# Kernel tuning notes

Hardware: AMD Instinct MI355X
Metric: run time of the kernel (lower is better)

The kernel has to match this reference:

```python
import math
import jax, jax.numpy as jnp
import numpy as np

NUM_EMBED = 2048
EMBED_FEATS = 64
IN_FEATS = 512
B, T = 16, 4096
COMMITMENT_COST = 0.25


def setup_inputs() -> dict:
    key = jax.random.key(0)
    k1, k2, k3, k4 = jax.random.split(key, 4)
    x = jax.random.normal(k1, (B, IN_FEATS, T), dtype=jnp.float32)
    proj_w = jax.random.normal(k2, (EMBED_FEATS, IN_FEATS), dtype=jnp.float32) / np.sqrt(IN_FEATS)
    proj_b = jax.random.normal(k3, (EMBED_FEATS,), dtype=jnp.float32) * 0.01
    embed = jax.random.normal(k4, (NUM_EMBED, EMBED_FEATS), dtype=jnp.float32)
    return {"x": x, "proj_w": proj_w, "proj_b": proj_b, "embed": embed}


def reference(x, proj_w, proj_b, embed):
    # 1x1 Conv1d projection, then transpose(1,-1): [B, Cin, T] -> [B, T, E]
    h = jnp.einsum('ec,bct->bte', proj_w, x) + proj_b  # [B, T, E]
    Bb, Tt, E = h.shape
    K = embed.shape[0]
    flat = h.reshape(-1, E)  # [N, E]
    # squared distances to codewords: [N, K]
    d2 = (jnp.sum(flat * flat, axis=1, keepdims=True)
          + jnp.sum(embed * embed, axis=1)
          - 2.0 * flat @ embed.T)
    q_idx = jnp.argmin(d2, axis=1)  # [N]
    z_q = embed[q_idx].reshape(Bb, Tt, E)  # one-hot @ embed == gather
    # commitment loss (codebook updated by EMA, so only commitment term)
    commitment = jnp.mean((jax.lax.stop_gradient(z_q) - h) ** 2)
    loss = COMMITMENT_COST * commitment
    # straight-through estimator
    z_q_st = h + jax.lax.stop_gradient(z_q - h)
    # code usage stats
    N = flat.shape[0]
    probs = jnp.zeros((K,), dtype=jnp.float32).at[q_idx].add(1.0) / N
    log_perplexity = -jnp.sum(probs * jnp.log(probs + 1e-10))
    kldiv_r = math.log(K) * (N / Bb) * jnp.ones((Bb, 1), dtype=jnp.float32)
    z_q_out = jnp.swapaxes(z_q_st, 1, 2)  # [B, E, T]
    return z_q_out, loss, kldiv_r, log_perplexity
```

## Files before the change

kernel.cpp:

```cpp
#include <hip/hip_runtime.h>
#include <math.h>

#define B_ 16
#define T_ 4096
#define C_ 512
#define E_ 64
#define K_ 2048
#define N_ (B_*T_)
#define ZQ_ELEMS 4194304

typedef __attribute__((ext_vector_type(8))) short short8;
typedef __attribute__((ext_vector_type(4))) short short4v;
typedef __attribute__((ext_vector_type(4))) float f32x4;

#define WS_EHI   0
#define WS_ELO   262144
#define WS_NHCC  524288
#define WS_WHI   532480
#define WS_WLO   598016
#define WS_QIDX  663552
#define WS_HIST  925696
#define WS_LOSS  933888

struct HiLo { short hi, lo; };

__device__ __forceinline__ unsigned short rne16(float v) {
    unsigned u = __float_as_uint(v);
    return (unsigned short)((u + 0x7FFFu + ((u >> 16) & 1u)) >> 16);
}
__device__ __forceinline__ HiLo split_rne(float v) {
    HiLo r;
    unsigned hb = rne16(v);
    r.hi = (short)hb;
    float hf = __uint_as_float((unsigned)hb << 16);
    r.lo = (short)rne16(v - hf);
    return r;
}

__global__ void prep_kernel(const float* __restrict__ embed,
                            const float* __restrict__ W,
                            short* __restrict__ ehi, short* __restrict__ elo,
                            float* __restrict__ nhcc,
                            short* __restrict__ whi, short* __restrict__ wlo) {
    const int tid = threadIdx.x;
    if (blockIdx.x < 64) {
        const int row = blockIdx.x * 32 + (tid >> 3);
        const int c = (tid & 7) * 8;
        const float* src = embed + (size_t)row * 64 + c;
        short8 hv, lv;
        float s = 0.f;
#pragma unroll
        for (int j = 0; j < 8; ++j) {
            float v = src[j];
            s = fmaf(v, v, s);
            HiLo r = split_rne(v);
            hv[j] = r.hi; lv[j] = r.lo;
        }
        *(short8*)(ehi + (size_t)row * 64 + c) = hv;
        *(short8*)(elo + (size_t)row * 64 + c) = lv;
        s += __shfl_xor(s, 1, 64);
        s += __shfl_xor(s, 2, 64);
        s += __shfl_xor(s, 4, 64);
        if ((tid & 7) == 0) nhcc[row] = -0.5f * s;
    } else {
        int idx = ((blockIdx.x - 64) * 256 + tid) * 4;
        float4 v = *(const float4*)(W + idx);
        short4v h, l;
        HiLo a = split_rne(v.x); h[0] = a.hi; l[0] = a.lo;
        HiLo b = split_rne(v.y); h[1] = b.hi; l[1] = b.lo;
        HiLo c = split_rne(v.z); h[2] = c.hi; l[2] = c.lo;
        HiLo d = split_rne(v.w); h[3] = d.hi; l[3] = d.lo;
        *(short4v*)(whi + idx) = h;
        *(short4v*)(wlo + idx) = l;
    }
}

__global__ __launch_bounds__(256, 2) void projvq_kernel(
        const float* __restrict__ x,
        const short* __restrict__ whi, const short* __restrict__ wlo,
        const float* __restrict__ bias,
        const short* __restrict__ ehi, const short* __restrict__ elo,
        const float* __restrict__ nhcc,
        int* __restrict__ qidx, int* __restrict__ hist,
        float* __restrict__ lossacc) {
    __shared__ float smemf[8704];
    float* xs = smemf;
    short* hT_hi = (short*)smemf;
    short* hT_lo = hT_hi + 8704;
    short* es_hi = (short*)smemf;
    short* es_lo = es_hi + 8192;
    float* ccs   = (float*)(es_lo + 8192);

    const int tid = threadIdx.x;
    const int wave = tid >> 6, lane = tid & 63;
    const int row16 = lane & 15, quad = lane >> 4;
    const int n0 = blockIdx.x * 128;
    const int b  = n0 / T_;
    const int t0 = n0 % T_;
    const float* xb = x + (size_t)b * C_ * T_ + t0;

    f32x4 acc[2][4];
#pragma unroll
    for (int i = 0; i < 2; ++i)
#pragma unroll
        for (int j = 0; j < 4; ++j) acc[i][j] = (f32x4){0.f, 0.f, 0.f, 0.f};

    for (int c0 = 0; c0 < C_; c0 += 32) {
#pragma unroll
        for (int j = 0; j < 4; ++j) {
            int linear = j * 1024 + tid * 4;
            int cc = linear >> 7, tt = linear & 127;
            float4 v = *(const float4*)(xb + (size_t)(c0 + cc) * T_ + tt);
            *(float4*)(xs + cc * 136 + tt) = v;
        }
        __syncthreads();

        short8 bh[2], bl[2];
#pragma unroll
        for (int tt2 = 0; tt2 < 2; ++tt2) {
            int t = wave * 32 + tt2 * 16 + row16;
#pragma unroll
            for (int j = 0; j < 8; ++j) {
                float v = xs[(quad * 8 + j) * 136 + t];
                HiLo r = split_rne(v);
                bh[tt2][j] = r.hi; bl[tt2][j] = r.lo;
            }
        }

#pragma unroll
        for (int et = 0; et < 4; ++et) {
            size_t aoff = (size_t)(et * 16 + row16) * C_ + c0 + quad * 8;
            short8 ah = *(const short8*)(whi + aoff);
            short8 al = *(const short8*)(wlo + aoff);
#pragma unroll
            for (int tt2 = 0; tt2 < 2; ++tt2) {
                acc[tt2][et] = __builtin_amdgcn_mfma_f32_16x16x32_bf16(ah, bh[tt2], acc[tt2][et], 0, 0, 0);
                acc[tt2][et] = __builtin_amdgcn_mfma_f32_16x16x32_bf16(al, bh[tt2], acc[tt2][et], 0, 0, 0);
                acc[tt2][et] = __builtin_amdgcn_mfma_f32_16x16x32_bf16(ah, bl[tt2], acc[tt2][et], 0, 0, 0);
                acc[tt2][et] = __builtin_amdgcn_mfma_f32_16x16x32_bf16(al, bl[tt2], acc[tt2][et], 0, 0, 0);
            }
        }
        __syncthreads();
    }

    float hh = 0.f;
#pragma unroll
    for (int et = 0; et < 4; ++et) {
        float4 bv = *(const float4*)(bias + et * 16 + quad * 4);
#pragma unroll
        for (int tt2 = 0; tt2 < 2; ++tt2) {
            f32x4 a = acc[tt2][et];
            a[0] += bv.x; a[1] += bv.y; a[2] += bv.z; a[3] += bv.w;
            hh = fmaf(a[0], a[0], hh); hh = fmaf(a[1], a[1], hh);
            hh = fmaf(a[2], a[2], hh); hh = fmaf(a[3], a[3], hh);
            short4v hv, lv;
#pragma unroll
            for (int r = 0; r < 4; ++r) {
                HiLo sp = split_rne(a[r]);
                hv[r] = sp.hi; lv[r] = sp.lo;
            }
            int t = wave * 32 + tt2 * 16 + row16;
            int e0 = et * 16 + quad * 4;
            *(short4v*)(hT_hi + t * 68 + e0) = hv;
            *(short4v*)(hT_lo + t * 68 + e0) = lv;
        }
    }
#pragma unroll
    for (int m = 1; m < 64; m <<= 1) hh += __shfl_xor(hh, m, 64);
    if (lane == 0) atomicAdd(lossacc, hh);
    __syncthreads();

    short8 a_hi[2][2], a_lo[2][2];
#pragma unroll
    for (int rt = 0; rt < 2; ++rt)
#pragma unroll
        for (int ks = 0; ks < 2; ++ks) {
            int lr = wave * 32 + rt * 16 + row16;
            a_hi[rt][ks] = *(const short8*)(hT_hi + lr * 68 + ks * 32 + quad * 8);
            a_lo[rt][ks] = *(const short8*)(hT_lo + lr * 68 + ks * 32 + quad * 8);
        }
    __syncthreads();

    const int rs = row16 & 7;
    const int off0 = (quad ^ rs) * 8;

    float vmax[2][4];
    int   vidx[2][4];
#pragma unroll
    for (int rt = 0; rt < 2; ++rt)
#pragma unroll
        for (int rg = 0; rg < 4; ++rg) { vmax[rt][rg] = -3.4e38f; vidx[rt][rg] = 0; }

    for (int k0 = 0; k0 < K_; k0 += 128) {
#pragma unroll
        for (int it = 0; it < 4; ++it) {
            int idx = it * 256 + tid;
            int r = idx >> 3, g = idx & 7;
            int dst = r * 64 + (g ^ (r & 7)) * 8;
            *(short8*)(es_hi + dst) = *(const short8*)(ehi + (size_t)(k0 + r) * 64 + g * 8);
            *(short8*)(es_lo + dst) = *(const short8*)(elo + (size_t)(k0 + r) * 64 + g * 8);
        }
        if (tid < 32) *(f32x4*)(ccs + tid * 4) = *(const f32x4*)(nhcc + k0 + tid * 4);
        __syncthreads();

#pragma unroll
        for (int kt = 0; kt < 8; ++kt) {
            const int row = kt * 16 + row16;
            const float ci = ccs[row];
            const short* p = es_hi + row * 64;
            const short* q = es_lo + row * 64;
            short8 bh0 = *(const short8*)(p + off0);
            short8 bh1 = *(const short8*)(p + (off0 ^ 32));
            short8 bl0 = *(const short8*)(q + off0);
            short8 bl1 = *(const short8*)(q + (off0 ^ 32));
            const int kk = k0 + row;
#pragma unroll
            for (int rt = 0; rt < 2; ++rt) {
                f32x4 acc2 = {ci, ci, ci, ci};
                acc2 = __builtin_amdgcn_mfma_f32_16x16x32_bf16(a_hi[rt][0], bh0, acc2, 0, 0, 0);
                acc2 = __builtin_amdgcn_mfma_f32_16x16x32_bf16(a_hi[rt][1], bh1, acc2, 0, 0, 0);
                acc2 = __builtin_amdgcn_mfma_f32_16x16x32_bf16(a_lo[rt][0], bh0, acc2, 0, 0, 0);
                acc2 = __builtin_amdgcn_mfma_f32_16x16x32_bf16(a_lo[rt][1], bh1, acc2, 0, 0, 0);
                acc2 = __builtin_amdgcn_mfma_f32_16x16x32_bf16(a_hi[rt][0], bl0, acc2, 0, 0, 0);
                acc2 = __builtin_amdgcn_mfma_f32_16x16x32_bf16(a_hi[rt][1], bl1, acc2, 0, 0, 0);
#pragma unroll
                for (int rg = 0; rg < 4; ++rg) {
                    float v = acc2[rg];
                    if (v > vmax[rt][rg]) { vmax[rt][rg] = v; vidx[rt][rg] = kk; }
                }
            }
        }
        __syncthreads();
    }

    float s = 0.f;
#pragma unroll
    for (int rt = 0; rt < 2; ++rt) {
#pragma unroll
        for (int rg = 0; rg < 4; ++rg) {
            float v = vmax[rt][rg];
            int ix = vidx[rt][rg];
#pragma unroll
            for (int m = 1; m < 16; m <<= 1) {
                float ov = __shfl_xor(v, m, 64);
                int   oi = __shfl_xor(ix, m, 64);
                if (ov > v || (ov == v && oi < ix)) { v = ov; ix = oi; }
            }
            if (row16 == 0) {
                int rown = n0 + wave * 32 + rt * 16 + quad * 4 + rg;
                qidx[rown] = ix;
                atomicAdd(&hist[ix], 1);
                s += v;
            }
        }
    }
    s += __shfl_xor(s, 16, 64);
    s += __shfl_xor(s, 32, 64);
    if (lane == 0) atomicAdd(lossacc, -2.f * s);
}

__global__ void gather_kernel(const float* __restrict__ embed,
                              const int* __restrict__ qidx,
                              float* __restrict__ out) {
    __shared__ float tile[64 * 65];
    __shared__ int qs[64];
    const int tid = threadIdx.x;
    const int t0 = blockIdx.x * 64;
    const int b  = blockIdx.y;

    if (tid < 64) qs[tid] = qidx[b * T_ + t0 + tid];
    __syncthreads();

    const int t_l = tid >> 2, eq = tid & 3;
    const float4* src = (const float4*)(embed + (size_t)qs[t_l] * 64 + eq * 16);
#pragma unroll
    for (int j = 0; j < 4; ++j) {
        float4 v = src[j];
        int e = eq * 16 + j * 4;
        tile[t_l * 65 + e + 0] = v.x;
        tile[t_l * 65 + e + 1] = v.y;
        tile[t_l * 65 + e + 2] = v.z;
        tile[t_l * 65 + e + 3] = v.w;
    }
    __syncthreads();

    const int tt = tid & 63;
#pragma unroll
    for (int j = 0; j < 16; ++j) {
        int e = j * 4 + (tid >> 6);
        out[((size_t)b * 64 + e) * T_ + t0 + tt] = tile[tt * 65 + e];
    }
}

__global__ void finalize_kernel(const int* __restrict__ hist,
                                const float* __restrict__ lossacc,
                                float* __restrict__ out) {
    __shared__ float red[4];
    const int tid = threadIdx.x;
    float s = 0.f;
    for (int k = tid; k < K_; k += 256) {
        float p = (float)hist[k] * (1.f / 65536.f);
        s -= p * logf(p + 1e-10f);
    }
#pragma unroll
    for (int m = 1; m < 64; m <<= 1) s += __shfl_xor(s, m, 64);
    if ((tid & 63) == 0) red[tid >> 6] = s;
    __syncthreads();
    if (tid == 0) {
        float lp = red[0] + red[1] + red[2] + red[3];
        out[ZQ_ELEMS] = 0.25f * lossacc[0] / (float)ZQ_ELEMS;
        out[ZQ_ELEMS + 17] = lp;
    }
    if (tid < 16) out[ZQ_ELEMS + 1 + tid] = logf(2048.f) * 4096.f;
}

extern "C" void kernel_launch(void* const* d_in, const int* in_sizes, int n_in,
                              void* d_out, int out_size, void* d_ws, size_t ws_size,
                              hipStream_t stream) {
    const float* x      = (const float*)d_in[0];
    const float* proj_w = (const float*)d_in[1];
    const float* proj_b = (const float*)d_in[2];
    const float* embed  = (const float*)d_in[3];
    float* out = (float*)d_out;
    char* ws = (char*)d_ws;

    short* e_hi = (short*)(ws + WS_EHI);
    short* e_lo = (short*)(ws + WS_ELO);
    float* nhcc = (float*)(ws + WS_NHCC);
    short* w_hi = (short*)(ws + WS_WHI);
    short* w_lo = (short*)(ws + WS_WLO);
    int*   qidx = (int*)(ws + WS_QIDX);
    int*   hist = (int*)(ws + WS_HIST);
    float* lossac = (float*)(ws + WS_LOSS);

    (void)hipMemsetAsync(ws + WS_HIST, 0, K_ * sizeof(int) + sizeof(float), stream);

    prep_kernel<<<96, 256, 0, stream>>>(embed, proj_w, e_hi, e_lo, nhcc, w_hi, w_lo);
    projvq_kernel<<<N_ / 128, 256, 0, stream>>>(x, w_hi, w_lo, proj_b,
                                                e_hi, e_lo, nhcc, qidx, hist, lossac);
    gather_kernel<<<dim3(T_ / 64, B_), 256, 0, stream>>>(embed, qidx, out);
    finalize_kernel<<<1, 256, 0, stream>>>(hist, lossac, out);
}
```

Before: 309.1 us.

## Fuse codebook gather into VQ kernel and prefetch x and codebook tiles

Folds the gather/transpose of chosen codewords into the projection+VQ kernel, so the separate gather launch and the qidx round-trip through global memory go away. The codebook hi/lo copies are stored pre-permuted in MFMA fragment order, so the shared-memory fill and fragment reads become linear. Codebook chunks and x tiles are software-prefetched into registers one iteration ahead to overlap global loads with MFMA work. The bias/norm constant is now added after the MFMA chain. The trade-off is higher register pressure in a kernel launched with two blocks per SM, plus a longer kernel tail.

Result: no change. 305.5 us (-1.2%).

```diff
diff --git a/kernel.cpp b/kernel.cpp
--- a/kernel.cpp
+++ b/kernel.cpp
@@ -18,9 +18,8 @@
 #define WS_NHCC  524288
 #define WS_WHI   532480
 #define WS_WLO   598016
-#define WS_QIDX  663552
-#define WS_HIST  925696
-#define WS_LOSS  933888
+#define WS_HIST  663552
+#define WS_LOSS  671744
 
 struct HiLo { short hi, lo; };
 
@@ -45,8 +44,8 @@
     const int tid = threadIdx.x;
     if (blockIdx.x < 64) {
         const int row = blockIdx.x * 32 + (tid >> 3);
-        const int c = (tid & 7) * 8;
-        const float* src = embed + (size_t)row * 64 + c;
+        const int g = tid & 7;
+        const float* src = embed + (size_t)row * 64 + g * 8;
         short8 hv, lv;
         float s = 0.f;
 #pragma unroll
@@ -56,12 +55,15 @@
             HiLo r = split_rne(v);
             hv[j] = r.hi; lv[j] = r.lo;
         }
-        *(short8*)(ehi + (size_t)row * 64 + c) = hv;
-        *(short8*)(elo + (size_t)row * 64 + c) = lv;
+        const int c128 = row >> 7, r = row & 127;
+        const int kt = r >> 4, col = r & 15, ks = g >> 2, qe = g & 3;
+        const int slot = (kt * 2 + ks) * 64 + qe * 16 + col;
+        *(short8*)(ehi + c128 * 8192 + slot * 8) = hv;
+        *(short8*)(elo + c128 * 8192 + slot * 8) = lv;
         s += __shfl_xor(s, 1, 64);
         s += __shfl_xor(s, 2, 64);
         s += __shfl_xor(s, 4, 64);
-        if ((tid & 7) == 0) nhcc[row] = -0.5f * s;
+        if (g == 0) nhcc[row] = -0.5f * s;
     } else {
         int idx = ((blockIdx.x - 64) * 256 + tid) * 4;
         float4 v = *(const float4*)(W + idx);
@@ -81,39 +83,49 @@
         const float* __restrict__ bias,
         const short* __restrict__ ehi, const short* __restrict__ elo,
         const float* __restrict__ nhcc,
-        int* __restrict__ qidx, int* __restrict__ hist,
-        float* __restrict__ lossacc) {
-    __shared__ float smemf[8704];
-    float* xs = smemf;
-    short* hT_hi = (short*)smemf;
-    short* hT_lo = hT_hi + 8704;
-    short* es_hi = (short*)smemf;
-    short* es_lo = es_hi + 8192;
-    float* ccs   = (float*)(es_lo + 8192);
+        const float* __restrict__ embed, float* __restrict__ out,
+        int* __restrict__ hist, float* __restrict__ lossacc) {
+    __shared__ float smemf[8832];
+    float* xs   = smemf;
+    short* aimg = (short*)smemf;
+    short* es   = (short*)smemf;
+    float* ccs  = (float*)(smemf + 8192);
+    float* tile = smemf;
+    __shared__ int qs[128];
 
     const int tid = threadIdx.x;
     const int wave = tid >> 6, lane = tid & 63;
     const int row16 = lane & 15, quad = lane >> 4;
-    const int n0 = blockIdx.x * 128;
-    const int b  = n0 / T_;
-    const int t0 = n0 % T_;
+    const int b  = blockIdx.x >> 5;
+    const int t0 = (blockIdx.x & 31) * 128;
     const float* xb = x + (size_t)b * C_ * T_ + t0;
 
+    f32x4 cc0 = *(const f32x4*)(nhcc + tid * 8);
+    f32x4 cc1 = *(const f32x4*)(nhcc + tid * 8 + 4);
+
     f32x4 acc[2][4];
 #pragma unroll
     for (int i = 0; i < 2; ++i)
 #pragma unroll
         for (int j = 0; j < 4; ++j) acc[i][j] = (f32x4){0.f, 0.f, 0.f, 0.f};
 
+    const int xcc = tid >> 5;
+    const int xtt = (tid & 31) * 4;
+    float4 xpf[4];
+#pragma unroll
+    for (int j = 0; j < 4; ++j)
+        xpf[j] = *(const float4*)(xb + (size_t)(xcc + j * 8) * T_ + xtt);
+
     for (int c0 = 0; c0 < C_; c0 += 32) {
 #pragma unroll
-        for (int j = 0; j < 4; ++j) {
-            int linear = j * 1024 + tid * 4;
-            int cc = linear >> 7, tt = linear & 127;
-            float4 v = *(const float4*)(xb + (size_t)(c0 + cc) * T_ + tt);
-            *(float4*)(xs + cc * 136 + tt) = v;
-        }
+        for (int j = 0; j < 4; ++j)
+            *(float4*)(xs + (xcc + j * 8) * 136 + xtt) = xpf[j];
         __syncthreads();
+        if (c0 < C_ - 32) {
+#pragma unroll
+            for (int j = 0; j < 4; ++j)
+                xpf[j] = *(const float4*)(xb + (size_t)(c0 + 32 + xcc + j * 8) * T_ + xtt);
+        }
 
         short8 bh[2], bl[2];
 #pragma unroll
@@ -126,7 +138,6 @@
                 bh[tt2][j] = r.hi; bl[tt2][j] = r.lo;
             }
         }
-
 #pragma unroll
         for (int et = 0; et < 4; ++et) {
             size_t aoff = (size_t)(et * 16 + row16) * C_ + c0 + quad * 8;
@@ -159,10 +170,12 @@
                 HiLo sp = split_rne(a[r]);
                 hv[r] = sp.hi; lv[r] = sp.lo;
             }
-            int t = wave * 32 + tt2 * 16 + row16;
-            int e0 = et * 16 + quad * 4;
-            *(short4v*)(hT_hi + t * 68 + e0) = hv;
-            *(short4v*)(hT_lo + t * 68 + e0) = lv;
+            const int ks = et >> 1;
+            const int qe = (et & 1) * 2 + (quad >> 1);
+            const int j0 = (quad & 1) * 4;
+            const int sl = (((wave * 2 + tt2) * 2 + ks) * 64 + qe * 16 + row16) * 8 + j0;
+            *(short4v*)(aimg + sl) = hv;
+            *(short4v*)(aimg + 8192 + sl) = lv;
         }
     }
 #pragma unroll
@@ -175,14 +188,18 @@
     for (int rt = 0; rt < 2; ++rt)
 #pragma unroll
         for (int ks = 0; ks < 2; ++ks) {
-            int lr = wave * 32 + rt * 16 + row16;
-            a_hi[rt][ks] = *(const short8*)(hT_hi + lr * 68 + ks * 32 + quad * 8);
-            a_lo[rt][ks] = *(const short8*)(hT_lo + lr * 68 + ks * 32 + quad * 8);
-        }
-    __syncthreads();
-
-    const int rs = row16 & 7;
-    const int off0 = (quad ^ rs) * 8;
+            int sl = (((wave * 2 + rt) * 2 + ks) * 64 + lane) * 8;
+            a_hi[rt][ks] = *(const short8*)(aimg + sl);
+            a_lo[rt][ks] = *(const short8*)(aimg + 8192 + sl);
+        }
+    __syncthreads();
+
+    short8 pf[8];
+#pragma unroll
+    for (int it = 0; it < 4; ++it) {
+        pf[it]     = *(const short8*)(ehi + (it * 256 + tid) * 8);
+        pf[4 + it] = *(const short8*)(elo + (it * 256 + tid) * 8);
+    }
 
     float vmax[2][4];
     int   vidx[2][4];
@@ -191,41 +208,49 @@
 #pragma unroll
         for (int rg = 0; rg < 4; ++rg) { vmax[rt][rg] = -3.4e38f; vidx[rt][rg] = 0; }
 
-    for (int k0 = 0; k0 < K_; k0 += 128) {
+    for (int c = 0; c < 16; ++c) {
 #pragma unroll
         for (int it = 0; it < 4; ++it) {
-            int idx = it * 256 + tid;
-            int r = idx >> 3, g = idx & 7;
-            int dst = r * 64 + (g ^ (r & 7)) * 8;
-            *(short8*)(es_hi + dst) = *(const short8*)(ehi + (size_t)(k0 + r) * 64 + g * 8);
-            *(short8*)(es_lo + dst) = *(const short8*)(elo + (size_t)(k0 + r) * 64 + g * 8);
-        }
-        if (tid < 32) *(f32x4*)(ccs + tid * 4) = *(const f32x4*)(nhcc + k0 + tid * 4);
+            *(short8*)(es + (it * 256 + tid) * 8)        = pf[it];
+            *(short8*)(es + 8192 + (it * 256 + tid) * 8) = pf[4 + it];
+        }
+        if ((tid >> 4) == c) {
+            int u = tid & 15;
+            *(f32x4*)(ccs + u * 8)     = cc0;
+            *(f32x4*)(ccs + u * 8 + 4) = cc1;
+        }
         __syncthreads();
+        if (c < 15) {
+            const short* sh = ehi + (c + 1) * 8192;
+            const short* sl2 = elo + (c + 1) * 8192;
+#pragma unroll
+            for (int it = 0; it < 4; ++it) {
+                pf[it]     = *(const short8*)(sh + (it * 256 + tid) * 8);
+                pf[4 + it] = *(const short8*)(sl2 + (it * 256 + tid) * 8);
+            }
+        }
 
 #pragma unroll
         for (int kt = 0; kt < 8; ++kt) {
-            const int row = kt * 16 + row16;
-            const float ci = ccs[row];
-            const short* p = es_hi + row * 64;
-            const short* q = es_lo + row * 64;
-            short8 bh0 = *(const short8*)(p + off0);
-            short8 bh1 = *(const short8*)(p + (off0 ^ 32));
-            short8 bl0 = *(const short8*)(q + off0);
-            short8 bl1 = *(const short8*)(q + (off0 ^ 32));
-            const int kk = k0 + row;
+            const float ci = ccs[kt * 16 + row16];
+            const short* pb = es + (kt * 2) * 512;
+            short8 bh0 = *(const short8*)(pb + lane * 8);
+            short8 bh1 = *(const short8*)(pb + 512 + lane * 8);
+            short8 bl0 = *(const short8*)(pb + 8192 + lane * 8);
+            short8 bl1 = *(const short8*)(pb + 8192 + 512 + lane * 8);
+            const int kk = c * 128 + kt * 16 + row16;
 #pragma unroll
             for (int rt = 0; rt < 2; ++rt) {
-                f32x4 acc2 = {ci, ci, ci, ci};
-                acc2 = __builtin_amdgcn_mfma_f32_16x16x32_bf16(a_hi[rt][0], bh0, acc2, 0, 0, 0);
-                acc2 = __builtin_amdgcn_mfma_f32_16x16x32_bf16(a_hi[rt][1], bh1, acc2, 0, 0, 0);
-                acc2 = __builtin_amdgcn_mfma_f32_16x16x32_bf16(a_lo[rt][0], bh0, acc2, 0, 0, 0);
-                acc2 = __builtin_amdgcn_mfma_f32_16x16x32_bf16(a_lo[rt][1], bh1, acc2, 0, 0, 0);
-                acc2 = __builtin_amdgcn_mfma_f32_16x16x32_bf16(a_hi[rt][0], bl0, acc2, 0, 0, 0);
-                acc2 = __builtin_amdgcn_mfma_f32_16x16x32_bf16(a_hi[rt][1], bl1, acc2, 0, 0, 0);
+                f32x4 a2 = {0.f, 0.f, 0.f, 0.f};
+                a2 = __builtin_amdgcn_mfma_f32_16x16x32_bf16(a_hi[rt][0], bh0, a2, 0, 0, 0);
+                a2 = __builtin_amdgcn_mfma_f32_16x16x32_bf16(a_hi[rt][1], bh1, a2, 0, 0, 0);
+                a2 = __builtin_amdgcn_mfma_f32_16x16x32_bf16(a_lo[rt][0], bh0, a2, 0, 0, 0);
+                a2 = __builtin_amdgcn_mfma_f32_16x16x32_bf16(a_lo[rt][1], bh1, a2, 0, 0, 0);
+                a2 = __builtin_amdgcn_mfma_f32_16x16x32_bf16(a_hi[rt][0], bl0, a2, 0, 0, 0);
+                a2 = __builtin_amdgcn_mfma_f32_16x16x32_bf16(a_hi[rt][1], bl1, a2, 0, 0, 0);
 #pragma unroll
                 for (int rg = 0; rg < 4; ++rg) {
-                    float v = acc2[rg];
+                    float v = a2[rg] + ci;
                     if (v > vmax[rt][rg]) { vmax[rt][rg] = v; vidx[rt][rg] = kk; }
                 }
             }
@@ -247,8 +272,7 @@
                 if (ov > v || (ov == v && oi < ix)) { v = ov; ix = oi; }
             }
             if (row16 == 0) {
-                int rown = n0 + wave * 32 + rt * 16 + quad * 4 + rg;
-                qidx[rown] = ix;
+                qs[wave * 32 + rt * 16 + quad * 4 + rg] = ix;
                 atomicAdd(&hist[ix], 1);
                 s += v;
             }
@@ -257,38 +281,28 @@
     s += __shfl_xor(s, 16, 64);
     s += __shfl_xor(s, 32, 64);
     if (lane == 0) atomicAdd(lossacc, -2.f * s);
-}
-
-__global__ void gather_kernel(const float* __restrict__ embed,
-                              const int* __restrict__ qidx,
-                              float* __restrict__ out) {
-    __shared__ float tile[64 * 65];
-    __shared__ int qs[64];
-    const int tid = threadIdx.x;
-    const int t0 = blockIdx.x * 64;
-    const int b  = blockIdx.y;
-
-    if (tid < 64) qs[tid] = qidx[b * T_ + t0 + tid];
-    __syncthreads();
-
-    const int t_l = tid >> 2, eq = tid & 3;
-    const float4* src = (const float4*)(embed + (size_t)qs[t_l] * 64 + eq * 16);
-#pragma unroll
-    for (int j = 0; j < 4; ++j) {
-        float4 v = src[j];
-        int e = eq * 16 + j * 4;
-        tile[t_l * 65 + e + 0] = v.x;
-        tile[t_l * 65 + e + 1] = v.y;
-        tile[t_l * 65 + e + 2] = v.z;
-        tile[t_l * 65 + e + 3] = v.w;
-    }
-    __syncthreads();
-
-    const int tt = tid & 63;
-#pragma unroll
-    for (int j = 0; j < 16; ++j) {
-        int e = j * 4 + (tid >> 6);
-        out[((size_t)b * 64 + e) * T_ + t0 + tt] = tile[tt * 65 + e];
+    __syncthreads();
+
+    {
+        const int r = tid >> 1, piece = tid & 1;
+        const float* src = embed + (size_t)qs[r] * 64 + piece * 32;
+#pragma unroll
+        for (int j = 0; j < 8; ++j) {
+            float4 v = *(const float4*)(src + j * 4);
+            *(float4*)(tile + r * 69 + piece * 32 + j * 4) = v;
+        }
+    }
+    __syncthreads();
+    {
+        const int tt = tid & 63;
+        const int eo = tid >> 6;
+        float* ob = out + ((size_t)b * 64) * T_ + t0;
+#pragma unroll
+        for (int j = 0; j < 16; ++j) {
+            int e = j * 4 + eo;
+            ob[(size_t)e * T_ + tt]      = tile[tt * 69 + e];
+            ob[(size_t)e * T_ + 64 + tt] = tile[(tt + 64) * 69 + e];
+        }
     }
 }
 
@@ -329,7 +343,6 @@
     float* nhcc = (float*)(ws + WS_NHCC);
     short* w_hi = (short*)(ws + WS_WHI);
     short* w_lo = (short*)(ws + WS_WLO);
-    int*   qidx = (int*)(ws + WS_QIDX);
     int*   hist = (int*)(ws + WS_HIST);
     float* lossac = (float*)(ws + WS_LOSS);
 
@@ -337,7 +350,7 @@
 
     prep_kernel<<<96, 256, 0, stream>>>(embed, proj_w, e_hi, e_lo, nhcc, w_hi, w_lo);
     projvq_kernel<<<N_ / 128, 256, 0, stream>>>(x, w_hi, w_lo, proj_b,
-                                                e_hi, e_lo, nhcc, qidx, hist, lossac);
-    gather_kernel<<<dim3(T_ / 64, B_), 256, 0, stream>>>(embed, qidx, out);
+                                                e_hi, e_lo, nhcc, embed, out,
+                                                hist, lossac);
     finalize_kernel<<<1, 256, 0, stream>>>(hist, lossac, out);
 }
```
